# Kernel tuning notes

Hardware: AMD Instinct MI355X
Metric: run time of the kernel (lower is better)

The kernel has to match this reference:

```python
import jax, jax.numpy as jnp
import numpy as np

DIM = 512
BATCH, SEQ = 4, 4096


def setup_inputs() -> dict:
    key = jax.random.key(0)
    kx, kq, kk, kv, ko = jax.random.split(key, 5)
    s = DIM ** -0.5  # fan-in style init scale for stability
    return {
        "x": jax.random.normal(kx, (BATCH, SEQ, DIM), dtype=jnp.float32),
        "Wq": jax.random.normal(kq, (DIM, DIM), dtype=jnp.float32) * s,
        "Wk": jax.random.normal(kk, (DIM, DIM), dtype=jnp.float32) * s,
        "Wv": jax.random.normal(kv, (DIM, DIM), dtype=jnp.float32) * s,
        "Wo": jax.random.normal(ko, (DIM, DIM), dtype=jnp.float32) * s,
    }


def reference(x, Wq, Wk, Wv, Wo):
    # x: [B, S, D]; projections (torch Linear, no bias -> x @ W here)
    q = jnp.einsum('bsd,dk->bsk', x, Wq)  # [B,S,K]
    k = jnp.einsum('bsd,dk->bsk', x, Wk)  # [B,S,K]
    v = jnp.einsum('bsd,dv->bsv', x, Wv)  # [B,S,V]

    # sequential recurrence: M_t = M_{t-1} + v_t k_t^T ; y_t = M_t q_t
    def step(M, qkv_t):
        q_t, k_t, v_t = qkv_t  # each [B, K] / [B, V]
        M = M + v_t[:, :, None] * k_t[:, None, :]  # [B, V, K]
        y_t = jnp.einsum('bvk,bk->bv', M, q_t)
        return M, y_t

    M0 = jnp.zeros((x.shape[0], Wv.shape[1], Wk.shape[1]), dtype=x.dtype)
    qT = jnp.swapaxes(q, 0, 1)  # [S,B,K]
    kT = jnp.swapaxes(k, 0, 1)
    vT = jnp.swapaxes(v, 0, 1)
    _, ys = jax.lax.scan(step, M0, (qT, kT, vT))  # ys: [S,B,V]
    y = jnp.swapaxes(ys, 0, 1)  # [B,S,V]
    return jnp.einsum('bsv,vd->bsd', y, Wo)
```

## Files before the change

kernel.cpp:

```cpp
#include <hip/hip_runtime.h>
#include <hip/hip_bf16.h>

typedef __attribute__((ext_vector_type(8))) short bf16x8;
typedef __attribute__((ext_vector_type(4))) float f32x4;

__device__ inline short f2bf(float f) {
    __hip_bfloat16 h = __float2bfloat16(f);
    short s;
    __builtin_memcpy(&s, &h, 2);
    return s;
}
__device__ inline float bf2f(short s) {
    unsigned int u = ((unsigned int)(unsigned short)s) << 16;
    float f;
    __builtin_memcpy(&f, &u, 4);
    return f;
}

__device__ inline void cp16_async(const void* g, void* l) {
    __builtin_amdgcn_global_load_lds(
        (const __attribute__((address_space(1))) void*)g,
        (__attribute__((address_space(3))) void*)l, 16, 0, 0);
}


__global__ void prep_kernel(const float* __restrict__ x, short* __restrict__ Xb,
                            const float* __restrict__ W0, const float* __restrict__ W1,
                            const float* __restrict__ W2, const float* __restrict__ W3,
                            short* __restrict__ W4T) {
    int bid = blockIdx.x;
    if (bid < 8192) {
        int i = bid * 256 + threadIdx.x;
        float4 f = ((const float4*)x)[i];
        union { short s[4]; int2 v; } u;
        u.s[0] = f2bf(f.x); u.s[1] = f2bf(f.y); u.s[2] = f2bf(f.z); u.s[3] = f2bf(f.w);
        ((int2*)Xb)[i] = u.v;
    } else {
        int i = (bid - 8192) * 256 + threadIdx.x;
        int w = i >> 18;
        int r = i & 262143;
        int n = r >> 9, k = r & 511;
        const float* W = (w == 0) ? W0 : (w == 1) ? W1 : (w == 2) ? W2 : W3;
        W4T[i] = f2bf(W[k * 512 + n]);
    }
}


#define LDS_DECL __shared__ short sm[4][8192]

__device__ inline void stage_tile(const short* __restrict__ A, int lda,
                                  const short* __restrict__ B, int ldb, int k0,
                                  short* sA, short* sB, int tid) {
#pragma unroll
    for (int j = 0; j < 4; ++j) {
        const int L = tid * 16 + j * 4096;
        const int row = L >> 7;
        const int cb = (L & 127) ^ ((row & 7) << 4);
        cp16_async(A + (size_t)row * lda + k0 + (cb >> 1), (char*)sA + L);
        cp16_async(B + (size_t)row * ldb + k0 + (cb >> 1), (char*)sB + L);
    }
}

__device__ inline void compute_tile(const short* sA, const short* sB, f32x4* acc,
                                    int wr, int wc, int lr, int quad) {
    const int sw = (lr & 7) << 3;
#pragma unroll
    for (int kk = 0; kk < 2; ++kk) {
        const int co = (kk * 32 + quad * 8) ^ sw;
        bf16x8 af[4], bfr[4];
#pragma unroll
        for (int i = 0; i < 4; ++i)
            af[i] = *(const bf16x8*)&sA[(wr + i * 16 + lr) * 64 + co];
#pragma unroll
        for (int j = 0; j < 4; ++j)
            bfr[j] = *(const bf16x8*)&sB[(wc + j * 16 + lr) * 64 + co];
#pragma unroll
        for (int i = 0; i < 4; ++i)
#pragma unroll
            for (int j = 0; j < 4; ++j)
                acc[i * 4 + j] = __builtin_amdgcn_mfma_f32_16x16x32_bf16(af[i], bfr[j], acc[i * 4 + j], 0, 0, 0);
    }
}

__device__ inline void kloop_pipe(const short* __restrict__ A, int lda,
                                  const short* __restrict__ B, int ldb, int Kd,
                                  f32x4* acc, short (*sm)[8192]) {
    const int tid = threadIdx.x, lane = tid & 63, wv = tid >> 6;
    const int quad = lane >> 4, lr = lane & 15;
    const int wr = (wv >> 1) * 64, wc = (wv & 1) * 64;
    const int NT = Kd >> 6;
    stage_tile(A, lda, B, ldb, 0, sm[0], sm[1], tid);
    __builtin_amdgcn_sched_barrier(0);
    asm volatile("s_waitcnt vmcnt(0)" ::: "memory");
    __builtin_amdgcn_sched_barrier(0);
    __builtin_amdgcn_s_barrier();
    __builtin_amdgcn_sched_barrier(0);
    for (int t = 0; t < NT; ++t) {
        const int cur = (t & 1) << 1;
        if (t + 1 < NT)
            stage_tile(A, lda, B, ldb, (t + 1) << 6, sm[cur ^ 2], sm[cur ^ 3], tid);
        __builtin_amdgcn_sched_barrier(0);
        compute_tile(sm[cur], sm[cur + 1], acc, wr, wc, lr, quad);
        __builtin_amdgcn_sched_barrier(0);
        asm volatile("s_waitcnt vmcnt(0)" ::: "memory");
        __builtin_amdgcn_sched_barrier(0);
        __builtin_amdgcn_s_barrier();
        __builtin_amdgcn_sched_barrier(0);
    }
}

__device__ inline void store_out(float* p, float v) { *p = v; }
__device__ inline void store_out(short* p, float v) { *p = f2bf(v); }

template <typename OutT>
__device__ inline void store_tile128(OutT* C, int ldc, const f32x4* acc) {
    const int lane = threadIdx.x & 63, wv = threadIdx.x >> 6;
    const int quad = lane >> 4, lr = lane & 15;
    const int wr = (wv >> 1) * 64, wc = (wv & 1) * 64;
#pragma unroll
    for (int i = 0; i < 4; ++i)
#pragma unroll
        for (int j = 0; j < 4; ++j)
#pragma unroll
            for (int r = 0; r < 4; ++r)
                store_out(&C[(size_t)(wr + i * 16 + quad * 4 + r) * ldc + wc + j * 16 + lr],
                          acc[i * 4 + j][r]);
}

__global__ __launch_bounds__(256, 2) void proj_all(const short* __restrict__ Xb,
                                                   const short* __restrict__ W4T,
                                                   short* __restrict__ Qb, short* __restrict__ Kb,
                                                   short* __restrict__ Vt, short* __restrict__ Kt) {
    LDS_DECL;
    f32x4 acc[16];
#pragma unroll
    for (int i = 0; i < 16; ++i) acc[i] = (f32x4){0.f, 0.f, 0.f, 0.f};
    const int bid = blockIdx.x;
    const int lane = threadIdx.x & 63, wv = threadIdx.x >> 6;
    const int quad = lane >> 4, lr = lane & 15;
    const int wr = (wv >> 1) * 64, wc = (wv & 1) * 64;
    if (bid < 1024) {
        const int mt = bid >> 3, by = bid & 7;
        const short* At = Xb + (size_t)mt * 128 * 512;
        const short* Bt = W4T + (size_t)by * 128 * 512;
        short* Ct = ((by < 4) ? Qb : Kb) + (size_t)mt * 128 * 512 + (by & 3) * 128;
        kloop_pipe(At, 512, Bt, 512, 512, acc, sm);
        store_tile128(Ct, 512, acc);
        if (by >= 4) {
            const int b = mt >> 5;
            const int t0b = (mt & 31) * 128;
            const int f0 = (by - 4) * 128;
#pragma unroll
            for (int i = 0; i < 4; ++i)
#pragma unroll
                for (int j = 0; j < 4; ++j) {
                    int f = f0 + wc + j * 16 + lr;
                    int tt0 = t0b + wr + i * 16 + quad * 4;
                    short tmp[4];
#pragma unroll
                    for (int r = 0; r < 4; ++r) tmp[r] = f2bf(acc[i * 4 + j][r]);
                    *(int2*)&Kt[((size_t)b * 512 + f) * 4096 + tt0] = *(const int2*)tmp;
                }
        }
    } else {
        const int r = bid - 1024;
        const int b = r & 3, tt = (r >> 2) & 31, ft = r >> 7;
        const short* At = W4T + (size_t)2 * 262144 + (size_t)ft * 128 * 512;
        const short* Bt = Xb + ((size_t)b * 4096 + tt * 128) * 512;
        short* Ct = Vt + (size_t)b * 512 * 4096 + (size_t)ft * 128 * 4096 + tt * 128;
        kloop_pipe(At, 512, Bt, 512, 512, acc, sm);
        store_tile128(Ct, 4096, acc);
    }
}


__global__ __launch_bounds__(256, 2) void phaseA(const short* __restrict__ Vt,
                                                 const short* __restrict__ Kt,
                                                 short* __restrict__ AM) {
    LDS_DECL;
    const int bc = blockIdx.z, b = bc >> 4, c = bc & 15;
    const short* Ap = Vt + ((size_t)b * 512 + blockIdx.x * 128) * 4096 + c * 256;
    const short* Bp = Kt + ((size_t)b * 512 + blockIdx.y * 128) * 4096 + c * 256;
    short* Cp = AM + (size_t)bc * 262144 + (size_t)blockIdx.x * 128 * 512 + blockIdx.y * 128;
    f32x4 acc[16];
#pragma unroll
    for (int i = 0; i < 16; ++i) acc[i] = (f32x4){0.f, 0.f, 0.f, 0.f};
    kloop_pipe(Ap, 4096, Bp, 4096, 256, acc, sm);
    store_tile128(Cp, 512, acc);
}

__global__ __launch_bounds__(256, 2) void scan_phaseS(short* __restrict__ AM,
                                                      const short* __restrict__ Q,
                                                      const short* __restrict__ K,
                                                      short* __restrict__ P) {
    LDS_DECL;
    if (blockIdx.x < 512) {
        int i = blockIdx.x * 256 + threadIdx.x;
        int b = i >> 15;
        int vk8 = i & 32767;
        size_t base = (size_t)b * 16 * 262144 + (size_t)vk8 * 8;
        float acc[8];
#pragma unroll
        for (int s = 0; s < 8; ++s) acc[s] = 0.f;
        for (int c = 0; c < 16; ++c) {
            short* p = AM + base + (size_t)c * 262144;
            short in8[8];
            *(int4*)in8 = *(const int4*)p;
            short out8[8];
#pragma unroll
            for (int s = 0; s < 8; ++s) out8[s] = f2bf(acc[s]);
            *(int4*)p = *(const int4*)out8;
#pragma unroll
            for (int s = 0; s < 8; ++s) acc[s] += bf2f(in8[s]);
        }
        return;
    }
    const int e = blockIdx.x - 512;
    const int bc = e >> 2, mt = e & 1, nt = (e >> 1) & 1;
    if (mt < nt) return;
    const int b = bc >> 4, c = bc & 15;
    short* Pt = P + (size_t)bc * 65536 + (size_t)mt * 128 * 256 + nt * 128;
    const short* Ap = Q + ((size_t)(b * 4096 + c * 256 + mt * 128)) * 512;
    const short* Bp = K + ((size_t)(b * 4096 + c * 256 + nt * 128)) * 512;
    f32x4 acc[16];
#pragma unroll
    for (int i = 0; i < 16; ++i) acc[i] = (f32x4){0.f, 0.f, 0.f, 0.f};
    kloop_pipe(Ap, 512, Bp, 512, 512, acc, sm);
    const int lane = threadIdx.x & 63, wv = threadIdx.x >> 6;
    const int quad = lane >> 4, lr = lane & 15;
    const int wr = (wv >> 1) * 64, wc = (wv & 1) * 64;
    const bool diag = (mt == nt);
#pragma unroll
    for (int i = 0; i < 4; ++i)
#pragma unroll
        for (int j = 0; j < 4; ++j)
#pragma unroll
            for (int r = 0; r < 4; ++r) {
                int t = wr + i * 16 + quad * 4 + r;
                int jj = wc + j * 16 + lr;
                float v = (!diag || jj <= t) ? acc[i * 4 + j][r] : 0.f;
                Pt[(size_t)t * 256 + jj] = f2bf(v);
            }
}

__global__ __launch_bounds__(256, 2) void phaseY(const short* __restrict__ Q,
                                                 const short* __restrict__ Mpre,
                                                 const short* __restrict__ P,
                                                 const short* __restrict__ Vt,
                                                 short* __restrict__ Y) {
    LDS_DECL;
    const int bc = blockIdx.z, b = bc >> 4, c = bc & 15;
    const int mt = blockIdx.x, nt = blockIdx.y;
    f32x4 acc[16];
#pragma unroll
    for (int i = 0; i < 16; ++i) acc[i] = (f32x4){0.f, 0.f, 0.f, 0.f};
    const short* Ai = Q + ((size_t)(b * 4096 + c * 256 + mt * 128)) * 512;
    const short* Bi = Mpre + (size_t)bc * 262144 + (size_t)nt * 128 * 512;
    kloop_pipe(Ai, 512, Bi, 512, 512, acc, sm);
    const short* Ap = P + (size_t)bc * 65536 + (size_t)mt * 128 * 256;
    const short* Bv = Vt + ((size_t)b * 512 + nt * 128) * 4096 + c * 256;
    kloop_pipe(Ap, 256, Bv, 4096, (mt + 1) * 128, acc, sm);
    short* Cp = Y + ((size_t)(b * 4096 + c * 256 + mt * 128)) * 512 + nt * 128;
    store_tile128(Cp, 512, acc);
}

template <typename OutT>
__global__ __launch_bounds__(256, 2) void gemm128(const short* __restrict__ A, int lda,
                                                  const short* __restrict__ B, int ldb,
                                                  OutT* __restrict__ C, int ldc, int Kd) {
    LDS_DECL;
    const short* At = A + (size_t)blockIdx.x * 128 * lda;
    const short* Bt = B + (size_t)blockIdx.y * 128 * ldb;
    OutT* Ct = C + (size_t)blockIdx.x * 128 * ldc + blockIdx.y * 128;
    f32x4 acc[16];
#pragma unroll
    for (int i = 0; i < 16; ++i) acc[i] = (f32x4){0.f, 0.f, 0.f, 0.f};
    kloop_pipe(At, lda, Bt, ldb, Kd, acc, sm);
    store_tile128(Ct, ldc, acc);
}


extern "C" void kernel_launch(void* const* d_in, const int* in_sizes, int n_in,
                              void* d_out, int out_size, void* d_ws, size_t ws_size,
                              hipStream_t stream) {
    const float* x  = (const float*)d_in[0];
    const float* Wq = (const float*)d_in[1];
    const float* Wk = (const float*)d_in[2];
    const float* Wv = (const float*)d_in[3];
    const float* Wo = (const float*)d_in[4];
    float* out = (float*)d_out;

    const size_t NTD = 16384 * 512;

    short* ws  = (short*)d_ws;
    short* Xb  = ws;
    short* Qb  = Xb + NTD;
    short* Kb  = Qb + NTD;
    short* Kt  = Kb + NTD;
    short* Vt  = Kt + NTD;
    short* P   = Vt + NTD;
    short* W4T = P + 4194304;
    short* AM  = W4T + 1048576;
    short* Yb  = Kb;

    short* WoT = W4T + 3 * 262144;

    prep_kernel<<<12288, 256, 0, stream>>>(x, Xb, Wq, Wk, Wv, Wo, W4T);
    proj_all<<<1536, 256, 0, stream>>>(Xb, W4T, Qb, Kb, Vt, Kt);
    phaseA<<<dim3(4, 4, 64), 256, 0, stream>>>(Vt, Kt, AM);
    scan_phaseS<<<768, 256, 0, stream>>>(AM, Qb, Kb, P);
    phaseY<<<dim3(2, 4, 64), 256, 0, stream>>>(Qb, AM, P, Vt, Yb);
    gemm128<float><<<dim3(128, 4), 256, 0, stream>>>(Yb, 512, WoT, 512, out, 512, 512);
}
```

Measured before the change: 224.1 us.

## Replace QKV projection with 256x256-tile GEMM kernel writing transposed K/V epilogues

Replaces the 128x128-tile projection kernel (1536 blocks, with V computed as a separate transposed GEMM) with a 256x256-tile, 512-thread GEMM over the concatenated Q/K/V weights (384 blocks). K and V transposes are now written directly from the epilogue, and a block-index swizzle is added to improve L2 reuse. Larger tiles cut redundant operand loads, but they use 128KB of LDS and more registers per block, which lowers occupancy and leaves fewer blocks to fill the CUs.

```diff
diff --git a/kernel.cpp b/kernel.cpp
--- a/kernel.cpp
+++ b/kernel.cpp
@@ -46,6 +46,121 @@
 }
 
 
+__device__ inline void stage256(const short* __restrict__ A, int lda,
+                                const short* __restrict__ B, int ldb, int k0,
+                                short* sA, short* sB, int tid) {
+#pragma unroll
+    for (int j = 0; j < 4; ++j) {
+        const int L = tid * 16 + j * 8192;
+        const int row = L >> 7;
+        const int cb = (L & 127) ^ ((row & 7) << 4);
+        cp16_async((const char*)(A + (size_t)row * lda + k0) + cb, (char*)sA + L);
+        cp16_async((const char*)(B + (size_t)row * ldb + k0) + cb, (char*)sB + L);
+    }
+}
+
+__device__ inline void compute256(const short* sA, const short* sB, f32x4 acc[8][4],
+                                  int aBase, int bBase, int lr, int quad) {
+    const int sw = (lr & 7) << 4;
+#pragma unroll
+    for (int kk = 0; kk < 2; ++kk) {
+        const int cb = (kk * 64 + quad * 16) ^ sw;
+        bf16x8 a[8], b[4];
+#pragma unroll
+        for (int m = 0; m < 8; ++m)
+            a[m] = *(const bf16x8*)((const char*)sA + (aBase + m * 16 + lr) * 128 + cb);
+#pragma unroll
+        for (int n = 0; n < 4; ++n)
+            b[n] = *(const bf16x8*)((const char*)sB + (bBase + n * 16 + lr) * 128 + cb);
+#pragma unroll
+        for (int m = 0; m < 8; ++m)
+#pragma unroll
+            for (int n = 0; n < 4; ++n)
+                acc[m][n] = __builtin_amdgcn_mfma_f32_16x16x32_bf16(a[m], b[n], acc[m][n], 0, 0, 0);
+    }
+}
+
+__device__ inline void gemm256(const short* __restrict__ A, int lda,
+                               const short* __restrict__ B, int ldb, int Kd,
+                               f32x4 acc[8][4],
+                               short* s0, short* s1, short* s2, short* s3) {
+    const int tid = threadIdx.x, lane = tid & 63, wv = tid >> 6;
+    const int lr = lane & 15, quad = lane >> 4;
+    const int aBase = (wv >> 2) * 128, bBase = (wv & 3) * 64;
+    const int NT = Kd >> 6;
+    stage256(A, lda, B, ldb, 0, s0, s1, tid);
+    __builtin_amdgcn_sched_barrier(0);
+    asm volatile("s_waitcnt vmcnt(0)" ::: "memory");
+    __builtin_amdgcn_sched_barrier(0);
+    __builtin_amdgcn_s_barrier();
+    __builtin_amdgcn_sched_barrier(0);
+    for (int t = 0; t < NT; ++t) {
+        const short* cA = (t & 1) ? s2 : s0;
+        const short* cB = (t & 1) ? s3 : s1;
+        if (t + 1 < NT)
+            stage256(A, lda, B, ldb, (t + 1) << 6,
+                     (t & 1) ? s0 : s2, (t & 1) ? s1 : s3, tid);
+        __builtin_amdgcn_sched_barrier(0);
+        compute256(cA, cB, acc, aBase, bBase, lr, quad);
+        __builtin_amdgcn_sched_barrier(0);
+        asm volatile("s_waitcnt vmcnt(0)" ::: "memory");
+        __builtin_amdgcn_sched_barrier(0);
+        __builtin_amdgcn_s_barrier();
+        __builtin_amdgcn_sched_barrier(0);
+    }
+}
+
+__global__ __launch_bounds__(512, 2) void proj_qkv(const short* __restrict__ Xb,
+                                                   const short* __restrict__ W4T,
+                                                   short* __restrict__ Qb, short* __restrict__ Kb,
+                                                   short* __restrict__ Vt, short* __restrict__ Kt) {
+    __shared__ short sA0[16384], sB0[16384], sA1[16384], sB1[16384];
+    const int bid = blockIdx.x;
+    const int swz = (bid & 7) * 48 + (bid >> 3);
+    const int mt = swz / 6, nt = swz % 6;
+    f32x4 acc[8][4];
+#pragma unroll
+    for (int m = 0; m < 8; ++m)
+#pragma unroll
+        for (int n = 0; n < 4; ++n) acc[m][n] = (f32x4){0.f, 0.f, 0.f, 0.f};
+    gemm256(Xb + (size_t)mt * 256 * 512, 512, W4T + (size_t)nt * 256 * 512, 512, 512,
+            acc, sA0, sB0, sA1, sB1);
+    const int lane = threadIdx.x & 63, wv = threadIdx.x >> 6;
+    const int wm = wv >> 2, wn = wv & 3;
+    const int lr = lane & 15, quad = lane >> 4;
+    const int pr = nt >> 1;
+    const int fl = ((nt & 1) << 8) + wn * 64;
+    const int tg0 = mt * 256 + wm * 128 + quad * 4;
+    if (pr < 2) {
+        short* C = pr ? Kb : Qb;
+#pragma unroll
+        for (int m = 0; m < 8; ++m)
+#pragma unroll
+            for (int n = 0; n < 4; ++n) {
+                const size_t base = (size_t)(tg0 + m * 16) * 512 + fl + n * 16 + lr;
+#pragma unroll
+                for (int r = 0; r < 4; ++r)
+                    C[base + (size_t)r * 512] = f2bf(acc[m][n][r]);
+            }
+    }
+    if (pr) {
+        short* T = (pr == 1) ? Kt : Vt;
+        const int b = tg0 >> 12;
+        const int tl0 = tg0 & 4095;
+#pragma unroll
+        for (int m = 0; m < 8; ++m)
+#pragma unroll
+            for (int n = 0; n < 4; ++n) {
+                const int f = fl + n * 16 + lr;
+                short tmp[4];
+#pragma unroll
+                for (int r = 0; r < 4; ++r) tmp[r] = f2bf(acc[m][n][r]);
+                *(int2*)&T[((size_t)b * 512 + f) * 4096 + tl0 + m * 16] = *(const int2*)tmp;
+            }
+    }
+}
+
+
 #define LDS_DECL __shared__ short sm[4][8192]
 
 __device__ inline void stage_tile(const short* __restrict__ A, int lda,
@@ -125,52 +240,6 @@
             for (int r = 0; r < 4; ++r)
                 store_out(&C[(size_t)(wr + i * 16 + quad * 4 + r) * ldc + wc + j * 16 + lr],
                           acc[i * 4 + j][r]);
-}
-
-__global__ __launch_bounds__(256, 2) void proj_all(const short* __restrict__ Xb,
-                                                   const short* __restrict__ W4T,
-                                                   short* __restrict__ Qb, short* __restrict__ Kb,
-                                                   short* __restrict__ Vt, short* __restrict__ Kt) {
-    LDS_DECL;
-    f32x4 acc[16];
-#pragma unroll
-    for (int i = 0; i < 16; ++i) acc[i] = (f32x4){0.f, 0.f, 0.f, 0.f};
-    const int bid = blockIdx.x;
-    const int lane = threadIdx.x & 63, wv = threadIdx.x >> 6;
-    const int quad = lane >> 4, lr = lane & 15;
-    const int wr = (wv >> 1) * 64, wc = (wv & 1) * 64;
-    if (bid < 1024) {
-        const int mt = bid >> 3, by = bid & 7;
-        const short* At = Xb + (size_t)mt * 128 * 512;
-        const short* Bt = W4T + (size_t)by * 128 * 512;
-        short* Ct = ((by < 4) ? Qb : Kb) + (size_t)mt * 128 * 512 + (by & 3) * 128;
-        kloop_pipe(At, 512, Bt, 512, 512, acc, sm);
-        store_tile128(Ct, 512, acc);
-        if (by >= 4) {
-            const int b = mt >> 5;
-            const int t0b = (mt & 31) * 128;
-            const int f0 = (by - 4) * 128;
-#pragma unroll
-            for (int i = 0; i < 4; ++i)
-#pragma unroll
-                for (int j = 0; j < 4; ++j) {
-                    int f = f0 + wc + j * 16 + lr;
-                    int tt0 = t0b + wr + i * 16 + quad * 4;
-                    short tmp[4];
-#pragma unroll
-                    for (int r = 0; r < 4; ++r) tmp[r] = f2bf(acc[i * 4 + j][r]);
-                    *(int2*)&Kt[((size_t)b * 512 + f) * 4096 + tt0] = *(const int2*)tmp;
-                }
-        }
-    } else {
-        const int r = bid - 1024;
-        const int b = r & 3, tt = (r >> 2) & 31, ft = r >> 7;
-        const short* At = W4T + (size_t)2 * 262144 + (size_t)ft * 128 * 512;
-        const short* Bt = Xb + ((size_t)b * 4096 + tt * 128) * 512;
-        short* Ct = Vt + (size_t)b * 512 * 4096 + (size_t)ft * 128 * 4096 + tt * 128;
-        kloop_pipe(At, 512, Bt, 512, 512, acc, sm);
-        store_tile128(Ct, 4096, acc);
-    }
 }
 
 
@@ -306,7 +375,7 @@
     short* WoT = W4T + 3 * 262144;
 
     prep_kernel<<<12288, 256, 0, stream>>>(x, Xb, Wq, Wk, Wv, Wo, W4T);
-    proj_all<<<1536, 256, 0, stream>>>(Xb, W4T, Qb, Kb, Vt, Kt);
+    proj_qkv<<<384, 512, 0, stream>>>(Xb, W4T, Qb, Kb, Vt, Kt);
     phaseA<<<dim3(4, 4, 64), 256, 0, stream>>>(Vt, Kt, AM);
     scan_phaseS<<<768, 256, 0, stream>>>(AM, Qb, Kb, P);
     phaseY<<<dim3(2, 4, 64), 256, 0, stream>>>(Qb, AM, P, Vt, Yb);
```

Result: slower. 231.5 us (+3.3%).

## Deepen GEMM k-loop pipeline to 4-stage ring with 32-wide k tiles

Applied to the files above, without the earlier changes.

Replaces the double-buffered 64-wide k-tile pipeline with a four-slot ring of 32-wide k tiles, keeping three tiles in flight. It waits with partial vmcnt counts instead of draining all loads each iteration. The goal is to hide global-to-LDS latency behind MFMA work. In exchange there are twice as many barriers per k step and a new 4-way LDS swizzle, with the same total LDS use.

```diff
diff --git a/kernel.cpp b/kernel.cpp
--- a/kernel.cpp
+++ b/kernel.cpp
@@ -46,63 +46,68 @@
 }
 
 
-#define LDS_DECL __shared__ short sm[4][8192]
-
-__device__ inline void stage_tile(const short* __restrict__ A, int lda,
-                                  const short* __restrict__ B, int ldb, int k0,
-                                  short* sA, short* sB, int tid) {
-#pragma unroll
-    for (int j = 0; j < 4; ++j) {
+#define LDS_DECL __shared__ short sm[8][4096]
+
+__device__ inline void stage32(const short* __restrict__ A, int lda,
+                               const short* __restrict__ B, int ldb, int k0,
+                               short* sA, short* sB, int tid) {
+#pragma unroll
+    for (int j = 0; j < 2; ++j) {
         const int L = tid * 16 + j * 4096;
-        const int row = L >> 7;
-        const int cb = (L & 127) ^ ((row & 7) << 4);
-        cp16_async(A + (size_t)row * lda + k0 + (cb >> 1), (char*)sA + L);
-        cp16_async(B + (size_t)row * ldb + k0 + (cb >> 1), (char*)sB + L);
-    }
-}
-
-__device__ inline void compute_tile(const short* sA, const short* sB, f32x4* acc,
-                                    int wr, int wc, int lr, int quad) {
-    const int sw = (lr & 7) << 3;
-#pragma unroll
-    for (int kk = 0; kk < 2; ++kk) {
-        const int co = (kk * 32 + quad * 8) ^ sw;
-        bf16x8 af[4], bfr[4];
-#pragma unroll
-        for (int i = 0; i < 4; ++i)
-            af[i] = *(const bf16x8*)&sA[(wr + i * 16 + lr) * 64 + co];
+        const int row = L >> 6;
+        const int cb = (L & 63) ^ ((row & 3) << 4);
+        cp16_async((const char*)(A + (size_t)row * lda + k0) + cb, (char*)sA + L);
+        cp16_async((const char*)(B + (size_t)row * ldb + k0) + cb, (char*)sB + L);
+    }
+}
+
+__device__ inline void compute32(const short* sA, const short* sB, f32x4* acc,
+                                 int wr, int wc, int lr, int quad) {
+    const int cb = (quad * 16) ^ ((lr & 3) << 4);
+    bf16x8 af[4], bfr[4];
+#pragma unroll
+    for (int i = 0; i < 4; ++i)
+        af[i] = *(const bf16x8*)((const char*)sA + (wr + i * 16 + lr) * 64 + cb);
+#pragma unroll
+    for (int j = 0; j < 4; ++j)
+        bfr[j] = *(const bf16x8*)((const char*)sB + (wc + j * 16 + lr) * 64 + cb);
+#pragma unroll
+    for (int i = 0; i < 4; ++i)
 #pragma unroll
         for (int j = 0; j < 4; ++j)
-            bfr[j] = *(const bf16x8*)&sB[(wc + j * 16 + lr) * 64 + co];
-#pragma unroll
-        for (int i = 0; i < 4; ++i)
-#pragma unroll
-            for (int j = 0; j < 4; ++j)
-                acc[i * 4 + j] = __builtin_amdgcn_mfma_f32_16x16x32_bf16(af[i], bfr[j], acc[i * 4 + j], 0, 0, 0);
-    }
+            acc[i * 4 + j] = __builtin_amdgcn_mfma_f32_16x16x32_bf16(af[i], bfr[j], acc[i * 4 + j], 0, 0, 0);
 }
 
 __device__ inline void kloop_pipe(const short* __restrict__ A, int lda,
                                   const short* __restrict__ B, int ldb, int Kd,
-                                  f32x4* acc, short (*sm)[8192]) {
+                                  f32x4* acc, short (*sm)[4096]) {
     const int tid = threadIdx.x, lane = tid & 63, wv = tid >> 6;
     const int quad = lane >> 4, lr = lane & 15;
     const int wr = (wv >> 1) * 64, wc = (wv & 1) * 64;
-    const int NT = Kd >> 6;
-    stage_tile(A, lda, B, ldb, 0, sm[0], sm[1], tid);
+    const int NT = Kd >> 5;
+    stage32(A, lda, B, ldb, 0,  sm[0], sm[1], tid);
+    stage32(A, lda, B, ldb, 32, sm[2], sm[3], tid);
+    stage32(A, lda, B, ldb, 64, sm[4], sm[5], tid);
     __builtin_amdgcn_sched_barrier(0);
-    asm volatile("s_waitcnt vmcnt(0)" ::: "memory");
+    asm volatile("s_waitcnt vmcnt(8)" ::: "memory");
     __builtin_amdgcn_sched_barrier(0);
     __builtin_amdgcn_s_barrier();
     __builtin_amdgcn_sched_barrier(0);
     for (int t = 0; t < NT; ++t) {
-        const int cur = (t & 1) << 1;
-        if (t + 1 < NT)
-            stage_tile(A, lda, B, ldb, (t + 1) << 6, sm[cur ^ 2], sm[cur ^ 3], tid);
+        const int cur = (t & 3) << 1;
+        if (t + 3 < NT)
+            stage32(A, lda, B, ldb, (t + 3) << 5,
+                    sm[((t + 3) & 3) << 1], sm[(((t + 3) & 3) << 1) + 1], tid);
         __builtin_amdgcn_sched_barrier(0);
-        compute_tile(sm[cur], sm[cur + 1], acc, wr, wc, lr, quad);
+        compute32(sm[cur], sm[cur + 1], acc, wr, wc, lr, quad);
         __builtin_amdgcn_sched_barrier(0);
-        asm volatile("s_waitcnt vmcnt(0)" ::: "memory");
+        if (t + 3 < NT) {
+            asm volatile("s_waitcnt vmcnt(8)" ::: "memory");
+        } else if (t + 2 < NT) {
+            asm volatile("s_waitcnt vmcnt(4)" ::: "memory");
+        } else {
+            asm volatile("s_waitcnt vmcnt(0)" ::: "memory");
+        }
         __builtin_amdgcn_sched_barrier(0);
         __builtin_amdgcn_s_barrier();
         __builtin_amdgcn_sched_barrier(0);
```

Measured after the change: 230.1 us. 2.7% more time.
